# Kernel optimization log

Measured on AMD Instinct MI355X. Metric: run time of the kernel, lower is better.

The kernel has to match this reference:

```python
import jax, jax.numpy as jnp
from jax import lax
import numpy as np

D_MODEL = 1024
D_STATE = 128
D_CONV = 4
EXPAND = 2
HEADDIM = 64
CHUNK = 10
D_INNER = EXPAND * D_MODEL          # 2048
NHEADS = D_INNER // HEADDIM         # 32
CONV_DIM = D_INNER + 2 * D_STATE    # 2304
BATCH, SEQ = 2, 1000


def setup_inputs() -> dict:
    key = jax.random.key(0)
    ks = jax.random.split(key, 9)
    n = lambda k, shp, sc: jax.random.normal(k, shp, dtype=jnp.float32) * sc
    return {
        "x": n(ks[0], (BATCH, SEQ, D_MODEL), 1.0),
        "W_in": n(ks[1], (2 * D_INNER + 2 * D_STATE + NHEADS, D_MODEL), 0.02),
        "conv_w": n(ks[2], (CONV_DIM, D_CONV), 0.2),
        "conv_b": n(ks[3], (CONV_DIM,), 0.02),
        "dt_bias": n(ks[4], (NHEADS,), 0.5),
        "A_log": jnp.log(jnp.linspace(1.0, 16.0, NHEADS)).astype(jnp.float32),
        "D": n(ks[6], (NHEADS,), 1.0),
        "norm_w": jnp.ones((D_INNER,), jnp.float32),
        "W_out": n(ks[8], (D_MODEL, D_INNER), 0.02),
    }


def segsum(x):
    # x: (..., T) -> (..., T, T) with out[i,j] = sum_{k=j+1..i} x_k for i>=j else -inf
    cs = jnp.cumsum(x, axis=-1)
    seg = cs[..., :, None] - cs[..., None, :]
    T = x.shape[-1]
    mask = jnp.tril(jnp.ones((T, T), bool))
    return jnp.where(mask, seg, -jnp.inf)


def ssd(x, A, Bm, Cm, chunk):
    # x: (b,l,h,p)  A: (b,l,h)  Bm,Cm: (b,l,n)  (ngroups=1, group dim squeezed)
    b, l, h, p = x.shape
    n = Bm.shape[-1]
    c = l // chunk
    xr = x.reshape(b, c, chunk, h, p)
    Ar = A.reshape(b, c, chunk, h).transpose(0, 3, 1, 2)      # (b,h,c,s)
    Br = Bm.reshape(b, c, chunk, n)
    Cr = Cm.reshape(b, c, chunk, n)
    Acs = jnp.cumsum(Ar, axis=-1)                              # (b,h,c,s)
    L = jnp.exp(segsum(Ar))                                    # (b,h,c,s,s)
    # intra-chunk (diagonal blocks)
    Y_diag = jnp.einsum('bcln,bcsn,bhcls,bcshp->bclhp', Cr, Br, L, xr)
    # per-chunk end states
    decay_states = jnp.exp(Acs[..., -1:] - Acs)                # (b,h,c,s)
    states = jnp.einsum('bcln,bhcl,bclhp->bchpn', Br, decay_states, xr)
    states = jnp.concatenate([jnp.zeros((b, 1, h, p, n), x.dtype), states], axis=1)
    # inter-chunk recurrence (parallel form)
    chunk_sums = jnp.pad(Acs[..., -1], ((0, 0), (0, 0), (1, 0)))  # (b,h,c+1)
    decay_chunk = jnp.exp(segsum(chunk_sums))                    # (b,h,c+1,c+1)
    new_states = jnp.einsum('bhzc,bchpn->bzhpn', decay_chunk, states)
    prev_states = new_states[:, :-1]                             # (b,c,h,p,n)
    # state -> output contribution
    Y_off = jnp.einsum('bcln,bchpn,bhcl->bclhp', Cr, prev_states, jnp.exp(Acs))
    return (Y_diag + Y_off).reshape(b, l, h, p)


def reference(x, W_in, conv_w, conv_b, dt_bias, A_log, D, norm_w, W_out):
    b, l, _ = x.shape
    zxbcdt = x @ W_in.T                                          # (b,l,4384)
    z = zxbcdt[..., :D_INNER]
    xBC = zxbcdt[..., D_INNER:D_INNER + CONV_DIM]
    dt = zxbcdt[..., D_INNER + CONV_DIM:]
    dt = jax.nn.softplus(dt + dt_bias)                           # (b,l,h)
    # causal depthwise conv1d
    xc = jnp.pad(xBC, ((0, 0), (D_CONV - 1, 0), (0, 0)))
    conv = lax.conv_general_dilated(
        xc.transpose(0, 2, 1), conv_w[:, None, :], (1,), 'VALID',
        feature_group_count=CONV_DIM,
        dimension_numbers=('NCH', 'OIH', 'NCH'))
    xBC = jax.nn.silu(conv.transpose(0, 2, 1) + conv_b)          # (b,l,conv_dim)
    x_ssm = xBC[..., :D_INNER].reshape(b, l, NHEADS, HEADDIM)
    Bm = xBC[..., D_INNER:D_INNER + D_STATE]
    Cm = xBC[..., D_INNER + D_STATE:]
    A = -jnp.exp(A_log)                                          # (h,)
    y = ssd(x_ssm * dt[..., None], A * dt, Bm, Cm, CHUNK)
    y = y + x_ssm * D[None, None, :, None]
    y = y.reshape(b, l, D_INNER)
    # gated RMSNorm
    y = y * jax.nn.silu(z)
    y = y * lax.rsqrt(jnp.mean(y * y, axis=-1, keepdims=True) + 1e-5) * norm_w
    return y @ W_out.T
```

## Files before the change

kernel.cpp:

```cpp
#include <hip/hip_runtime.h>
#include <hip/hip_bf16.h>

#define BATCHN 2
#define SEQL 1000
#define DMODEL 1024
#define DSTATE 128
#define HEADDIM 64
#define DINNER 2048
#define NHEADS 32
#define CONVDIM 2304
#define NPROJ 4384
#define TOKENS 2000
#define MPAD 2048
#define NPAD1 4480
#define QC 64
#define NCH 16

typedef __bf16 bfx8 __attribute__((ext_vector_type(8)));
typedef float fx4 __attribute__((ext_vector_type(4)));
typedef unsigned short u16x8 __attribute__((ext_vector_type(8)));

__device__ __forceinline__ unsigned short f2bf(float f) {
    unsigned int u = __builtin_bit_cast(unsigned int, f);
    u += 0x7FFFu + ((u >> 16) & 1u);
    return (unsigned short)(u >> 16);
}
__device__ __forceinline__ float bf2f(unsigned short u) {
    return __builtin_bit_cast(float, ((unsigned int)u) << 16);
}

__device__ __forceinline__ void gload16(const void* g, void* l) {
    __builtin_amdgcn_global_load_lds(
        (const __attribute__((address_space(1))) void*)g,
        (__attribute__((address_space(3))) void*)l, 16, 0, 0);
}

__global__ __launch_bounds__(256) void k_f2bf_pad(const float* __restrict__ src,
                                                  unsigned short* __restrict__ dst,
                                                  int n4src, int n4dst) {
    int i = blockIdx.x * 256 + threadIdx.x;
    if (i >= n4dst) return;
    ushort4 o = {0, 0, 0, 0};
    if (i < n4src) {
        float4 v = ((const float4*)src)[i];
        o.x = f2bf(v.x); o.y = f2bf(v.y); o.z = f2bf(v.z); o.w = f2bf(v.w);
    }
    ((ushort4*)dst)[i] = o;
}

__global__ __launch_bounds__(256) void k_dt(const float* __restrict__ x,
                                            const float* __restrict__ win,
                                            const float* __restrict__ dt_bias,
                                            float* __restrict__ dtv) {
    __shared__ float sx[8][1024];
    int t = threadIdx.x;
    int tok0 = blockIdx.x * 8;
    for (int i = t; i < 8 * 256; i += 256) {
        int tok = i >> 8, k4 = i & 255;
        ((float4*)&sx[tok][0])[k4] = ((const float4*)(x + (size_t)(tok0 + tok) * DMODEL))[k4];
    }
    __syncthreads();
    int tl = t >> 5, h = t & 31;
    const float4* wr_ = (const float4*)(win + (size_t)(2 * DINNER + 2 * DSTATE + h) * DMODEL);
    const float4* xr = (const float4*)&sx[tl][0];
    float acc = 0.f;
    #pragma unroll 4
    for (int k = 0; k < 256; ++k) {
        float4 a = xr[k], b = wr_[k];
        acc += a.x * b.x + a.y * b.y + a.z * b.z + a.w * b.w;
    }
    float v = acc + dt_bias[h];
    dtv[(size_t)(tok0 + tl) * NHEADS + h] = fmaxf(v, 0.f) + log1pf(expf(-fabsf(v)));
}

__global__ __launch_bounds__(256) void k_gemmd(const unsigned short* __restrict__ A,
                                               const unsigned short* __restrict__ B,
                                               float* __restrict__ C,
                                               int Mstore, int N, int K,
                                               int kc, size_t pstride) {
    __shared__ __attribute__((aligned(16))) unsigned short As[2][4096];
    __shared__ __attribute__((aligned(16))) unsigned short Bs[2][4096];
    int t = threadIdx.x;
    int lane = t & 63, wave = t >> 6;
    int wr = wave >> 1, wc = wave & 1;
    int m0 = blockIdx.y * 128, n0 = blockIdx.x * 128;
    int k0 = blockIdx.z * kc;
    int swcol = (((t & 3) ^ ((t >> 3) & 3)) * 8);
    const unsigned short* Ag = A + (size_t)(m0 + (t >> 2)) * K + k0 + swcol;
    const unsigned short* Bg = B + (size_t)(n0 + (t >> 2)) * K + k0 + swcol;
    int fr = lane & 15, ks = lane >> 4;
    int sl = (ks ^ ((fr >> 1) & 3)) << 3;
    fx4 acc[4][4] = {};
    gload16(Ag, &As[0][t * 8]);
    gload16(Ag + (size_t)64 * K, &As[0][2048 + t * 8]);
    gload16(Bg, &Bs[0][t * 8]);
    gload16(Bg + (size_t)64 * K, &Bs[0][2048 + t * 8]);
    __syncthreads();
    int cur = 0;
    for (int kk = 32; kk < kc; kk += 32) {
        gload16(Ag + kk, &As[cur ^ 1][t * 8]);
        gload16(Ag + (size_t)64 * K + kk, &As[cur ^ 1][2048 + t * 8]);
        gload16(Bg + kk, &Bs[cur ^ 1][t * 8]);
        gload16(Bg + (size_t)64 * K + kk, &Bs[cur ^ 1][2048 + t * 8]);
        bfx8 a[4], b[4];
        #pragma unroll
        for (int m = 0; m < 4; ++m)
            a[m] = *(const bfx8*)&As[cur][(wr * 64 + m * 16 + fr) * 32 + sl];
        #pragma unroll
        for (int n = 0; n < 4; ++n)
            b[n] = *(const bfx8*)&Bs[cur][(wc * 64 + n * 16 + fr) * 32 + sl];
        #pragma unroll
        for (int m = 0; m < 4; ++m)
            #pragma unroll
            for (int n = 0; n < 4; ++n)
                acc[m][n] = __builtin_amdgcn_mfma_f32_16x16x32_bf16(a[m], b[n], acc[m][n], 0, 0, 0);
        __syncthreads();
        cur ^= 1;
    }
    {
        bfx8 a[4], b[4];
        #pragma unroll
        for (int m = 0; m < 4; ++m)
            a[m] = *(const bfx8*)&As[cur][(wr * 64 + m * 16 + fr) * 32 + sl];
        #pragma unroll
        for (int n = 0; n < 4; ++n)
            b[n] = *(const bfx8*)&Bs[cur][(wc * 64 + n * 16 + fr) * 32 + sl];
        #pragma unroll
        for (int m = 0; m < 4; ++m)
            #pragma unroll
            for (int n = 0; n < 4; ++n)
                acc[m][n] = __builtin_amdgcn_mfma_f32_16x16x32_bf16(a[m], b[n], acc[m][n], 0, 0, 0);
    }
    float* Cz = C + (size_t)blockIdx.z * pstride;
    #pragma unroll
    for (int m = 0; m < 4; ++m) {
        int rbase = m0 + wr * 64 + m * 16 + (lane >> 4) * 4;
        #pragma unroll
        for (int i = 0; i < 4; ++i) {
            int r = rbase + i;
            if (r < Mstore) {
                #pragma unroll
                for (int n = 0; n < 4; ++n) {
                    int c = n0 + wc * 64 + n * 16 + fr;
                    if (c < N) Cz[(size_t)r * N + c] = acc[m][n][i];
                }
            }
        }
    }
}

__global__ __launch_bounds__(256) void k_red(const float* __restrict__ part,
                                             float* __restrict__ out, int n4, size_t pstride4) {
    int i = blockIdx.x * 256 + threadIdx.x;
    if (i >= n4) return;
    const float4* p = (const float4*)part;
    float4 v0 = p[i];
    float4 v1 = p[i + pstride4];
    float4 v2 = p[i + 2 * pstride4];
    float4 v3 = p[i + 3 * pstride4];
    float4 o;
    o.x = (v0.x + v1.x) + (v2.x + v3.x);
    o.y = (v0.y + v1.y) + (v2.y + v3.y);
    o.z = (v0.z + v1.z) + (v2.z + v3.z);
    o.w = (v0.w + v1.w) + (v2.w + v3.w);
    ((float4*)out)[i] = o;
}

__global__ __launch_bounds__(256) void k_conv4(const float* __restrict__ zx,
                                               const float* __restrict__ cw,
                                               const float* __restrict__ cb,
                                               float* __restrict__ xbc) {
    int idx = blockIdx.x * 256 + threadIdx.x;
    if (idx >= (TOKENS / 4) * CONVDIM) return;
    int tg = idx / CONVDIM;
    int col = idx - tg * CONVDIM;
    int b = tg / 250;
    int l0 = (tg - b * 250) * 4;
    float in[7];
    #pragma unroll
    for (int j = 0; j < 7; ++j) {
        int lj = l0 - 3 + j;
        in[j] = (lj >= 0) ? zx[(size_t)(b * SEQL + lj) * NPROJ + DINNER + col] : 0.f;
    }
    float w0 = cw[col * 4], w1 = cw[col * 4 + 1], w2 = cw[col * 4 + 2], w3 = cw[col * 4 + 3];
    float bb = cb[col];
    #pragma unroll
    for (int i = 0; i < 4; ++i) {
        float a = bb + w0 * in[i] + w1 * in[i + 1] + w2 * in[i + 2] + w3 * in[i + 3];
        xbc[(size_t)(b * SEQL + l0 + i) * CONVDIM + col] = a / (1.f + expf(-a));
    }
}

#define SCW 136
#define SWW 72
__global__ __launch_bounds__(256) void k_tile(const float* __restrict__ xbc,
                                              const float* __restrict__ dtv,
                                              const float* __restrict__ A_log,
                                              const float* __restrict__ Dp,
                                              float* __restrict__ ybuf,
                                              float* __restrict__ Sg,
                                              float* __restrict__ cumA) {
    __shared__ unsigned short sC[64 * SCW];
    __shared__ unsigned short sB[64 * SCW];
    __shared__ unsigned short sBdT[128 * SWW];
    __shared__ unsigned short sXdT[64 * SWW];
    __shared__ unsigned short sXr[64 * SWW];
    __shared__ float sAcs[64];
    __shared__ float sdt[64];
    int bid = blockIdx.x;
    int h = bid & 31;
    int tmp = bid >> 5;
    int c = tmp & 15;
    int b = tmp >> 4;
    size_t lin = (size_t)((b * NHEADS + h) * NCH + c);
    int t = threadIdx.x;
    int lane = t & 63, wave = t >> 6;
    if (t < 64) {
        int tok = c * QC + t;
        float d = (tok < SEQL) ? dtv[(size_t)(b * SEQL + tok) * NHEADS + h] : 0.f;
        float A = -expf(A_log[h]);
        float v = A * d;
        #pragma unroll
        for (int off = 1; off < 64; off <<= 1) {
            float u = __shfl_up(v, off, 64);
            if (lane >= off) v += u;
        }
        sdt[t] = d;
        sAcs[t] = v;
        cumA[lin * 64 + t] = v;
    }
    __syncthreads();
    float Aend = sAcs[63];
    for (int i = t; i < 64 * 32; i += 256) {
        int l = i >> 5, n4 = (i & 31) * 4;
        int tok = c * QC + l;
        float4 cv = {0, 0, 0, 0}, bv = {0, 0, 0, 0};
        if (tok < SEQL) {
            const float* base = xbc + (size_t)(b * SEQL + tok) * CONVDIM;
            bv = *(const float4*)(base + DINNER + n4);
            cv = *(const float4*)(base + DINNER + DSTATE + n4);
        }
        float dec = expf(Aend - sAcs[l]);
        sC[l * SCW + n4 + 0] = f2bf(cv.x); sC[l * SCW + n4 + 1] = f2bf(cv.y);
        sC[l * SCW + n4 + 2] = f2bf(cv.z); sC[l * SCW + n4 + 3] = f2bf(cv.w);
        sB[l * SCW + n4 + 0] = f2bf(bv.x); sB[l * SCW + n4 + 1] = f2bf(bv.y);
        sB[l * SCW + n4 + 2] = f2bf(bv.z); sB[l * SCW + n4 + 3] = f2bf(bv.w);
        sBdT[(n4 + 0) * SWW + l] = f2bf(bv.x * dec);
        sBdT[(n4 + 1) * SWW + l] = f2bf(bv.y * dec);
        sBdT[(n4 + 2) * SWW + l] = f2bf(bv.z * dec);
        sBdT[(n4 + 3) * SWW + l] = f2bf(bv.w * dec);
    }
    for (int i = t; i < 64 * 16; i += 256) {
        int l = i >> 4, p4 = (i & 15) * 4;
        int tok = c * QC + l;
        float4 xv = {0, 0, 0, 0};
        if (tok < SEQL) xv = *(const float4*)(xbc + (size_t)(b * SEQL + tok) * CONVDIM + h * 64 + p4);
        float d = sdt[l];
        sXr[l * SWW + p4 + 0] = f2bf(xv.x); sXr[l * SWW + p4 + 1] = f2bf(xv.y);
        sXr[l * SWW + p4 + 2] = f2bf(xv.z); sXr[l * SWW + p4 + 3] = f2bf(xv.w);
        sXdT[(p4 + 0) * SWW + l] = f2bf(xv.x * d);
        sXdT[(p4 + 1) * SWW + l] = f2bf(xv.y * d);
        sXdT[(p4 + 2) * SWW + l] = f2bf(xv.z * d);
        sXdT[(p4 + 3) * SWW + l] = f2bf(xv.w * d);
    }
    __syncthreads();
    int fr = lane & 15, fk8 = (lane >> 4) * 8;
    int wr = wave >> 1, wc = wave & 1;
    fx4 g[2][2] = {};
    #pragma unroll
    for (int k = 0; k < 4; ++k) {
        bfx8 a0 = *(const bfx8*)&sC[(wr * 32 + fr) * SCW + k * 32 + fk8];
        bfx8 a1 = *(const bfx8*)&sC[(wr * 32 + 16 + fr) * SCW + k * 32 + fk8];
        bfx8 b0 = *(const bfx8*)&sB[(wc * 32 + fr) * SCW + k * 32 + fk8];
        bfx8 b1 = *(const bfx8*)&sB[(wc * 32 + 16 + fr) * SCW + k * 32 + fk8];
        g[0][0] = __builtin_amdgcn_mfma_f32_16x16x32_bf16(a0, b0, g[0][0], 0, 0, 0);
        g[0][1] = __builtin_amdgcn_mfma_f32_16x16x32_bf16(a0, b1, g[0][1], 0, 0, 0);
        g[1][0] = __builtin_amdgcn_mfma_f32_16x16x32_bf16(a1, b0, g[1][0], 0, 0, 0);
        g[1][1] = __builtin_amdgcn_mfma_f32_16x16x32_bf16(a1, b1, g[1][1], 0, 0, 0);
    }
    __syncthreads();
    int rb = wr * 32 + (lane >> 4) * 4;
    int cb = wc * 32 + fr;
    #pragma unroll
    for (int m = 0; m < 2; ++m)
        #pragma unroll
        for (int n = 0; n < 2; ++n)
            #pragma unroll
            for (int i = 0; i < 4; ++i) {
                int row = rb + m * 16 + i, col = cb + n * 16;
                float wv = (col <= row) ? g[m][n][i] * expf(sAcs[row] - sAcs[col]) : 0.f;
                sB[row * SWW + col] = f2bf(wv);
            }
    __syncthreads();
    fx4 yd[2][2] = {};
    fx4 sc[2][4] = {};
    #pragma unroll
    for (int k = 0; k < 2; ++k) {
        bfx8 aW0 = *(const bfx8*)&sB[(wr * 32 + fr) * SWW + k * 32 + fk8];
        bfx8 aW1 = *(const bfx8*)&sB[(wr * 32 + 16 + fr) * SWW + k * 32 + fk8];
        bfx8 bX0 = *(const bfx8*)&sXdT[(wc * 32 + fr) * SWW + k * 32 + fk8];
        bfx8 bX1 = *(const bfx8*)&sXdT[(wc * 32 + 16 + fr) * SWW + k * 32 + fk8];
        yd[0][0] = __builtin_amdgcn_mfma_f32_16x16x32_bf16(aW0, bX0, yd[0][0], 0, 0, 0);
        yd[0][1] = __builtin_amdgcn_mfma_f32_16x16x32_bf16(aW0, bX1, yd[0][1], 0, 0, 0);
        yd[1][0] = __builtin_amdgcn_mfma_f32_16x16x32_bf16(aW1, bX0, yd[1][0], 0, 0, 0);
        yd[1][1] = __builtin_amdgcn_mfma_f32_16x16x32_bf16(aW1, bX1, yd[1][1], 0, 0, 0);
        bfx8 aX0 = *(const bfx8*)&sXdT[(wr * 32 + fr) * SWW + k * 32 + fk8];
        bfx8 aX1 = *(const bfx8*)&sXdT[(wr * 32 + 16 + fr) * SWW + k * 32 + fk8];
        #pragma unroll
        for (int j = 0; j < 4; ++j) {
            bfx8 bB = *(const bfx8*)&sBdT[(wc * 64 + j * 16 + fr) * SWW + k * 32 + fk8];
            sc[0][j] = __builtin_amdgcn_mfma_f32_16x16x32_bf16(aX0, bB, sc[0][j], 0, 0, 0);
            sc[1][j] = __builtin_amdgcn_mfma_f32_16x16x32_bf16(aX1, bB, sc[1][j], 0, 0, 0);
        }
    }
    float Dh = Dp[h];
    #pragma unroll
    for (int m = 0; m < 2; ++m)
        #pragma unroll
        for (int i = 0; i < 4; ++i) {
            int row = rb + m * 16 + i;
            int tok = c * QC + row;
            if (tok < SEQL) {
                #pragma unroll
                for (int n = 0; n < 2; ++n) {
                    int col = cb + n * 16;
                    float xr = bf2f(sXr[row * SWW + col]);
                    ybuf[(size_t)(b * SEQL + tok) * DINNER + h * 64 + col] = yd[m][n][i] + Dh * xr;
                }
            }
        }
    #pragma unroll
    for (int m = 0; m < 2; ++m)
        #pragma unroll
        for (int i = 0; i < 4; ++i) {
            int p = rb + m * 16 + i;
            #pragma unroll
            for (int j = 0; j < 4; ++j) {
                int n = wc * 64 + j * 16 + fr;
                Sg[lin * 8192 + p * 128 + n] = sc[m][j][i];
            }
        }
}

__global__ __launch_bounds__(256) void k_scan2v(float* __restrict__ Sg,
                                                const float* __restrict__ cumA) {
    int bid = blockIdx.x;
    int bh = bid >> 5, sub = bid & 31;
    int e = sub * 256 + threadIdx.x;
    __shared__ float sT[NCH];
    if (threadIdx.x < NCH)
        sT[threadIdx.x] = cumA[((size_t)(bh * NCH) + threadIdx.x) * 64 + 63];
    __syncthreads();
    float S = 0.f;
    size_t base = (size_t)bh * NCH * 8192 + e;
    for (int g = 0; g < NCH; ++g) {
        size_t off = base + (size_t)g * 8192;
        float sg = Sg[off];
        Sg[off] = S;
        S = expf(sT[g]) * S + sg;
    }
}

__global__ __launch_bounds__(256) void k_yoff(const float* __restrict__ xbc,
                                              const float* __restrict__ Sg,
                                              const float* __restrict__ cumA,
                                              float* __restrict__ ybuf) {
    int bid = blockIdx.x;
    int h = bid & 31;
    int tmp = bid >> 5;
    int c = tmp & 15;
    int b = tmp >> 4;
    if (c == 0) return;
    size_t lin = (size_t)((b * NHEADS + h) * NCH + c);
    __shared__ unsigned short sC[64 * SCW];
    __shared__ unsigned short sS[64 * SCW];
    __shared__ float sE[64];
    int t = threadIdx.x;
    int lane = t & 63, wave = t >> 6;
    if (t < 64) sE[t] = expf(cumA[lin * 64 + t]);
    for (int i = t; i < 64 * 32; i += 256) {
        int l = i >> 5, n4 = (i & 31) * 4;
        int tok = c * QC + l;
        float4 cv = {0, 0, 0, 0};
        if (tok < SEQL)
            cv = *(const float4*)(xbc + (size_t)(b * SEQL + tok) * CONVDIM + DINNER + DSTATE + n4);
        sC[l * SCW + n4 + 0] = f2bf(cv.x); sC[l * SCW + n4 + 1] = f2bf(cv.y);
        sC[l * SCW + n4 + 2] = f2bf(cv.z); sC[l * SCW + n4 + 3] = f2bf(cv.w);
        float4 sv = *(const float4*)(Sg + lin * 8192 + l * 128 + n4);
        sS[l * SCW + n4 + 0] = f2bf(sv.x); sS[l * SCW + n4 + 1] = f2bf(sv.y);
        sS[l * SCW + n4 + 2] = f2bf(sv.z); sS[l * SCW + n4 + 3] = f2bf(sv.w);
    }
    __syncthreads();
    int fr = lane & 15, fk8 = (lane >> 4) * 8;
    int wr = wave >> 1, wc = wave & 1;
    fx4 yo[2][2] = {};
    #pragma unroll
    for (int k = 0; k < 4; ++k) {
        bfx8 a0 = *(const bfx8*)&sC[(wr * 32 + fr) * SCW + k * 32 + fk8];
        bfx8 a1 = *(const bfx8*)&sC[(wr * 32 + 16 + fr) * SCW + k * 32 + fk8];
        bfx8 b0 = *(const bfx8*)&sS[(wc * 32 + fr) * SCW + k * 32 + fk8];
        bfx8 b1 = *(const bfx8*)&sS[(wc * 32 + 16 + fr) * SCW + k * 32 + fk8];
        yo[0][0] = __builtin_amdgcn_mfma_f32_16x16x32_bf16(a0, b0, yo[0][0], 0, 0, 0);
        yo[0][1] = __builtin_amdgcn_mfma_f32_16x16x32_bf16(a0, b1, yo[0][1], 0, 0, 0);
        yo[1][0] = __builtin_amdgcn_mfma_f32_16x16x32_bf16(a1, b0, yo[1][0], 0, 0, 0);
        yo[1][1] = __builtin_amdgcn_mfma_f32_16x16x32_bf16(a1, b1, yo[1][1], 0, 0, 0);
    }
    int rb = wr * 32 + (lane >> 4) * 4;
    int cb = wc * 32 + fr;
    #pragma unroll
    for (int m = 0; m < 2; ++m)
        #pragma unroll
        for (int i = 0; i < 4; ++i) {
            int row = rb + m * 16 + i;
            int tok = c * QC + row;
            if (tok < SEQL) {
                float e = sE[row];
                #pragma unroll
                for (int n = 0; n < 2; ++n) {
                    int col = cb + n * 16;
                    size_t off = (size_t)(b * SEQL + tok) * DINNER + h * 64 + col;
                    ybuf[off] += yo[m][n][i] * e;
                }
            }
        }
}

__global__ __launch_bounds__(256) void k_norm(const float* __restrict__ ybuf,
                                              const float* __restrict__ zx,
                                              const float* __restrict__ normw,
                                              unsigned short* __restrict__ ynb) {
    int row = blockIdx.x;
    int t = threadIdx.x;
    if (row >= TOKENS) {
        #pragma unroll
        for (int j = 0; j < 8; ++j) ynb[(size_t)row * DINNER + t + j * 256] = 0;
        return;
    }
    float v[8];
    float ss = 0.f;
    #pragma unroll
    for (int j = 0; j < 8; ++j) {
        int col = t + j * 256;
        float y = ybuf[(size_t)row * DINNER + col];
        float z = zx[(size_t)row * NPROJ + col];
        y *= z / (1.f + expf(-z));
        v[j] = y;
        ss += y * y;
    }
    #pragma unroll
    for (int off = 32; off > 0; off >>= 1) ss += __shfl_down(ss, off, 64);
    __shared__ float red[4];
    int lane = t & 63, wv = t >> 6;
    if (lane == 0) red[wv] = ss;
    __syncthreads();
    float tot = red[0] + red[1] + red[2] + red[3];
    float r = rsqrtf(tot * (1.f / DINNER) + 1e-5f);
    #pragma unroll
    for (int j = 0; j < 8; ++j) {
        int col = t + j * 256;
        ynb[(size_t)row * DINNER + col] = f2bf(v[j] * r * normw[col]);
    }
}

extern "C" void kernel_launch(void* const* d_in, const int* in_sizes, int n_in,
                              void* d_out, int out_size, void* d_ws, size_t ws_size,
                              hipStream_t stream) {
    const float* x       = (const float*)d_in[0];
    const float* W_in    = (const float*)d_in[1];
    const float* conv_w  = (const float*)d_in[2];
    const float* conv_b  = (const float*)d_in[3];
    const float* dt_bias = (const float*)d_in[4];
    const float* A_log   = (const float*)d_in[5];
    const float* Dp      = (const float*)d_in[6];
    const float* norm_w  = (const float*)d_in[7];
    const float* W_out   = (const float*)d_in[8];
    float* out = (float*)d_out;

    char* w = (char*)d_ws;
    auto alloc = [&](size_t bytes) {
        char* p = w;
        w += (bytes + 255) & ~(size_t)255;
        return p;
    };
    unsigned short* xb    = (unsigned short*)alloc((size_t)MPAD * DMODEL * 2);
    unsigned short* winb  = (unsigned short*)alloc((size_t)NPAD1 * DMODEL * 2);
    unsigned short* woutb = (unsigned short*)alloc((size_t)DMODEL * DINNER * 2);
    float* zx   = (float*)alloc((size_t)TOKENS * NPROJ * 4);
    float* xbc  = (float*)alloc((size_t)TOKENS * CONVDIM * 4);
    float* dtv  = (float*)alloc((size_t)TOKENS * NHEADS * 4);
    float* yb   = (float*)alloc((size_t)TOKENS * DINNER * 4);
    unsigned short* ynb = (unsigned short*)alloc((size_t)MPAD * DINNER * 2);
    float* Sg   = (float*)alloc((size_t)BATCHN * NHEADS * NCH * HEADDIM * DSTATE * 4);
    float* cumA = (float*)alloc((size_t)BATCHN * NHEADS * NCH * 64 * 4);

    int n4;
    n4 = MPAD * DMODEL / 4;
    k_f2bf_pad<<<(n4 + 255) / 256, 256, 0, stream>>>(x, xb, TOKENS * DMODEL / 4, n4);
    n4 = NPAD1 * DMODEL / 4;
    k_f2bf_pad<<<(n4 + 255) / 256, 256, 0, stream>>>(W_in, winb, NPROJ * DMODEL / 4, n4);
    n4 = DMODEL * DINNER / 4;
    k_f2bf_pad<<<(n4 + 255) / 256, 256, 0, stream>>>(W_out, woutb, n4, n4);
    k_dt<<<TOKENS / 8, 256, 0, stream>>>(x, W_in, dt_bias, dtv);
    dim3 g1(NPAD1 / 128, MPAD / 128, 1);
    k_gemmd<<<g1, 256, 0, stream>>>(xb, winb, zx, TOKENS, NPROJ, DMODEL, DMODEL, 0);
    k_conv4<<<(TOKENS / 4) * CONVDIM / 256, 256, 0, stream>>>(zx, conv_w, conv_b, xbc);
    k_tile<<<BATCHN * NHEADS * NCH, 256, 0, stream>>>(xbc, dtv, A_log, Dp, yb, Sg, cumA);
    k_scan2v<<<BATCHN * NHEADS * 32, 256, 0, stream>>>(Sg, cumA);
    k_yoff<<<BATCHN * NHEADS * NCH, 256, 0, stream>>>(xbc, Sg, cumA, yb);
    k_norm<<<MPAD, 256, 0, stream>>>(yb, zx, norm_w, ynb);
    size_t pstride = (size_t)MPAD * DMODEL;
    dim3 g2(DMODEL / 128, MPAD / 128, 4);
    k_gemmd<<<g2, 256, 0, stream>>>(ynb, woutb, zx, MPAD, DMODEL, DINNER, DINNER / 4, pstride);
    n4 = TOKENS * DMODEL / 4;
    k_red<<<(n4 + 255) / 256, 256, 0, stream>>>(zx, out, n4, pstride / 4);
}
```

Before: 186.5 us.

## Replace split-K output GEMM with 64-row tile GEMM and merge conversion kernels

```diff
diff --git a/kernel.cpp b/kernel.cpp
--- a/kernel.cpp
+++ b/kernel.cpp
@@ -35,17 +35,41 @@
         (__attribute__((address_space(3))) void*)l, 16, 0, 0);
 }
 
-__global__ __launch_bounds__(256) void k_f2bf_pad(const float* __restrict__ src,
-                                                  unsigned short* __restrict__ dst,
-                                                  int n4src, int n4dst) {
-    int i = blockIdx.x * 256 + threadIdx.x;
-    if (i >= n4dst) return;
-    ushort4 o = {0, 0, 0, 0};
-    if (i < n4src) {
-        float4 v = ((const float4*)src)[i];
-        o.x = f2bf(v.x); o.y = f2bf(v.y); o.z = f2bf(v.z); o.w = f2bf(v.w);
-    }
-    ((ushort4*)dst)[i] = o;
+#define N4_X   (MPAD * DMODEL / 4)
+#define N4_WIN (NPAD1 * DMODEL / 4)
+#define N4_WO  (DMODEL * DINNER / 4)
+__global__ __launch_bounds__(256) void k_f2bf3(const float* __restrict__ x,
+                                               const float* __restrict__ win,
+                                               const float* __restrict__ wout,
+                                               unsigned short* __restrict__ xb,
+                                               unsigned short* __restrict__ winb,
+                                               unsigned short* __restrict__ woutb) {
+    const int total = N4_X + N4_WIN + N4_WO;
+    for (int i = blockIdx.x * 256 + threadIdx.x; i < total; i += gridDim.x * 256) {
+        const float4* src;
+        ushort4* dst;
+        bool pad = false;
+        if (i < N4_X) {
+            pad = (i >= TOKENS * DMODEL / 4);
+            src = ((const float4*)x) + i;
+            dst = ((ushort4*)xb) + i;
+        } else if (i < N4_X + N4_WIN) {
+            int j = i - N4_X;
+            pad = (j >= NPROJ * DMODEL / 4);
+            src = ((const float4*)win) + j;
+            dst = ((ushort4*)winb) + j;
+        } else {
+            int j = i - N4_X - N4_WIN;
+            src = ((const float4*)wout) + j;
+            dst = ((ushort4*)woutb) + j;
+        }
+        ushort4 o = {0, 0, 0, 0};
+        if (!pad) {
+            float4 v = *src;
+            o.x = f2bf(v.x); o.y = f2bf(v.y); o.z = f2bf(v.z); o.w = f2bf(v.w);
+        }
+        *dst = o;
+    }
 }
 
 __global__ __launch_bounds__(256) void k_dt(const float* __restrict__ x,
@@ -76,18 +100,16 @@
 __global__ __launch_bounds__(256) void k_gemmd(const unsigned short* __restrict__ A,
                                                const unsigned short* __restrict__ B,
                                                float* __restrict__ C,
-                                               int Mstore, int N, int K,
-                                               int kc, size_t pstride) {
+                                               int Mstore, int N, int K) {
     __shared__ __attribute__((aligned(16))) unsigned short As[2][4096];
     __shared__ __attribute__((aligned(16))) unsigned short Bs[2][4096];
     int t = threadIdx.x;
     int lane = t & 63, wave = t >> 6;
     int wr = wave >> 1, wc = wave & 1;
     int m0 = blockIdx.y * 128, n0 = blockIdx.x * 128;
-    int k0 = blockIdx.z * kc;
     int swcol = (((t & 3) ^ ((t >> 3) & 3)) * 8);
-    const unsigned short* Ag = A + (size_t)(m0 + (t >> 2)) * K + k0 + swcol;
-    const unsigned short* Bg = B + (size_t)(n0 + (t >> 2)) * K + k0 + swcol;
+    const unsigned short* Ag = A + (size_t)(m0 + (t >> 2)) * K + swcol;
+    const unsigned short* Bg = B + (size_t)(n0 + (t >> 2)) * K + swcol;
     int fr = lane & 15, ks = lane >> 4;
     int sl = (ks ^ ((fr >> 1) & 3)) << 3;
     fx4 acc[4][4] = {};
@@ -97,7 +119,7 @@
     gload16(Bg + (size_t)64 * K, &Bs[0][2048 + t * 8]);
     __syncthreads();
     int cur = 0;
-    for (int kk = 32; kk < kc; kk += 32) {
+    for (int kk = 32; kk < K; kk += 32) {
         gload16(Ag + kk, &As[cur ^ 1][t * 8]);
         gload16(Ag + (size_t)64 * K + kk, &As[cur ^ 1][2048 + t * 8]);
         gload16(Bg + kk, &Bs[cur ^ 1][t * 8]);
@@ -131,7 +153,6 @@
             for (int n = 0; n < 4; ++n)
                 acc[m][n] = __builtin_amdgcn_mfma_f32_16x16x32_bf16(a[m], b[n], acc[m][n], 0, 0, 0);
     }
-    float* Cz = C + (size_t)blockIdx.z * pstride;
     #pragma unroll
     for (int m = 0; m < 4; ++m) {
         int rbase = m0 + wr * 64 + m * 16 + (lane >> 4) * 4;
@@ -142,28 +163,82 @@
                 #pragma unroll
                 for (int n = 0; n < 4; ++n) {
                     int c = n0 + wc * 64 + n * 16 + fr;
-                    if (c < N) Cz[(size_t)r * N + c] = acc[m][n][i];
+                    if (c < N) C[(size_t)r * N + c] = acc[m][n][i];
                 }
             }
         }
     }
 }
 
-__global__ __launch_bounds__(256) void k_red(const float* __restrict__ part,
-                                             float* __restrict__ out, int n4, size_t pstride4) {
-    int i = blockIdx.x * 256 + threadIdx.x;
-    if (i >= n4) return;
-    const float4* p = (const float4*)part;
-    float4 v0 = p[i];
-    float4 v1 = p[i + pstride4];
-    float4 v2 = p[i + 2 * pstride4];
-    float4 v3 = p[i + 3 * pstride4];
-    float4 o;
-    o.x = (v0.x + v1.x) + (v2.x + v3.x);
-    o.y = (v0.y + v1.y) + (v2.y + v3.y);
-    o.z = (v0.z + v1.z) + (v2.z + v3.z);
-    o.w = (v0.w + v1.w) + (v2.w + v3.w);
-    ((float4*)out)[i] = o;
+__global__ __launch_bounds__(256) void k_gemmB(const unsigned short* __restrict__ A,
+                                               const unsigned short* __restrict__ B,
+                                               float* __restrict__ C,
+                                               int Mstore, int N, int K) {
+    __shared__ __attribute__((aligned(16))) unsigned short As[2][2048];
+    __shared__ __attribute__((aligned(16))) unsigned short Bs[2][4096];
+    int t = threadIdx.x;
+    int lane = t & 63, wave = t >> 6;
+    int wr = wave >> 1, wc = wave & 1;
+    int m0 = blockIdx.y * 64, n0 = blockIdx.x * 128;
+    int swcol = (((t & 3) ^ ((t >> 3) & 3)) * 8);
+    const unsigned short* Ag = A + (size_t)(m0 + (t >> 2)) * K + swcol;
+    const unsigned short* Bg = B + (size_t)(n0 + (t >> 2)) * K + swcol;
+    int fr = lane & 15, ks = lane >> 4;
+    int sl = (ks ^ ((fr >> 1) & 3)) << 3;
+    fx4 acc[2][4] = {};
+    gload16(Ag, &As[0][t * 8]);
+    gload16(Bg, &Bs[0][t * 8]);
+    gload16(Bg + (size_t)64 * K, &Bs[0][2048 + t * 8]);
+    __syncthreads();
+    int cur = 0;
+    for (int kk = 32; kk < K; kk += 32) {
+        gload16(Ag + kk, &As[cur ^ 1][t * 8]);
+        gload16(Bg + kk, &Bs[cur ^ 1][t * 8]);
+        gload16(Bg + (size_t)64 * K + kk, &Bs[cur ^ 1][2048 + t * 8]);
+        bfx8 a[2], b[4];
+        #pragma unroll
+        for (int m = 0; m < 2; ++m)
+            a[m] = *(const bfx8*)&As[cur][(wr * 32 + m * 16 + fr) * 32 + sl];
+        #pragma unroll
+        for (int n = 0; n < 4; ++n)
+            b[n] = *(const bfx8*)&Bs[cur][(wc * 64 + n * 16 + fr) * 32 + sl];
+        #pragma unroll
+        for (int m = 0; m < 2; ++m)
+            #pragma unroll
+            for (int n = 0; n < 4; ++n)
+                acc[m][n] = __builtin_amdgcn_mfma_f32_16x16x32_bf16(a[m], b[n], acc[m][n], 0, 0, 0);
+        __syncthreads();
+        cur ^= 1;
+    }
+    {
+        bfx8 a[2], b[4];
+        #pragma unroll
+        for (int m = 0; m < 2; ++m)
+            a[m] = *(const bfx8*)&As[cur][(wr * 32 + m * 16 + fr) * 32 + sl];
+        #pragma unroll
+        for (int n = 0; n < 4; ++n)
+            b[n] = *(const bfx8*)&Bs[cur][(wc * 64 + n * 16 + fr) * 32 + sl];
+        #pragma unroll
+        for (int m = 0; m < 2; ++m)
+            #pragma unroll
+            for (int n = 0; n < 4; ++n)
+                acc[m][n] = __builtin_amdgcn_mfma_f32_16x16x32_bf16(a[m], b[n], acc[m][n], 0, 0, 0);
+    }
+    #pragma unroll
+    for (int m = 0; m < 2; ++m) {
+        int rbase = m0 + wr * 32 + m * 16 + (lane >> 4) * 4;
+        #pragma unroll
+        for (int i = 0; i < 4; ++i) {
+            int r = rbase + i;
+            if (r < Mstore) {
+                #pragma unroll
+                for (int n = 0; n < 4; ++n) {
+                    int c = n0 + wc * 64 + n * 16 + fr;
+                    C[(size_t)r * N + c] = acc[m][n][i];
+                }
+            }
+        }
+    }
 }
 
 __global__ __launch_bounds__(256) void k_conv4(const float* __restrict__ zx,
@@ -493,24 +568,15 @@
     float* Sg   = (float*)alloc((size_t)BATCHN * NHEADS * NCH * HEADDIM * DSTATE * 4);
     float* cumA = (float*)alloc((size_t)BATCHN * NHEADS * NCH * 64 * 4);
 
-    int n4;
-    n4 = MPAD * DMODEL / 4;
-    k_f2bf_pad<<<(n4 + 255) / 256, 256, 0, stream>>>(x, xb, TOKENS * DMODEL / 4, n4);
-    n4 = NPAD1 * DMODEL / 4;
-    k_f2bf_pad<<<(n4 + 255) / 256, 256, 0, stream>>>(W_in, winb, NPROJ * DMODEL / 4, n4);
-    n4 = DMODEL * DINNER / 4;
-    k_f2bf_pad<<<(n4 + 255) / 256, 256, 0, stream>>>(W_out, woutb, n4, n4);
+    k_f2bf3<<<2048, 256, 0, stream>>>(x, W_in, W_out, xb, winb, woutb);
     k_dt<<<TOKENS / 8, 256, 0, stream>>>(x, W_in, dt_bias, dtv);
-    dim3 g1(NPAD1 / 128, MPAD / 128, 1);
-    k_gemmd<<<g1, 256, 0, stream>>>(xb, winb, zx, TOKENS, NPROJ, DMODEL, DMODEL, 0);
+    dim3 g1(NPAD1 / 128, MPAD / 128);
+    k_gemmd<<<g1, 256, 0, stream>>>(xb, winb, zx, TOKENS, NPROJ, DMODEL);
     k_conv4<<<(TOKENS / 4) * CONVDIM / 256, 256, 0, stream>>>(zx, conv_w, conv_b, xbc);
     k_tile<<<BATCHN * NHEADS * NCH, 256, 0, stream>>>(xbc, dtv, A_log, Dp, yb, Sg, cumA);
     k_scan2v<<<BATCHN * NHEADS * 32, 256, 0, stream>>>(Sg, cumA);
     k_yoff<<<BATCHN * NHEADS * NCH, 256, 0, stream>>>(xbc, Sg, cumA, yb);
     k_norm<<<MPAD, 256, 0, stream>>>(yb, zx, norm_w, ynb);
-    size_t pstride = (size_t)MPAD * DMODEL;
-    dim3 g2(DMODEL / 128, MPAD / 128, 4);
-    k_gemmd<<<g2, 256, 0, stream>>>(ynb, woutb, zx, MPAD, DMODEL, DINNER, DINNER / 4, pstride);
-    n4 = TOKENS * DMODEL / 4;
-    k_red<<<(n4 + 255) / 256, 256, 0, stream>>>(zx, out, n4, pstride / 4);
-}
+    dim3 g2(DMODEL / 128, MPAD / 64);
+    k_gemmB<<<g2, 256, 0, stream>>>(ynb, woutb, out, TOKENS, DMODEL, DINNER);
+}
```

Result: no change. 183.1 us (-1.8%).
